# Kernel tuning notes

Hardware: AMD Instinct MI355X
Metric: run time of the kernel (lower is better)

The kernel has to match this reference:

```python
import jax, jax.numpy as jnp
import numpy as np

DIM = 2048
KV_DIM = 1024
NUM_HEADS = 16
HEAD_DIM = DIM // NUM_HEADS  # 128
EPS = 1e-6
B, LQ, LKV = 2, 4096, 1024


def _rope_cos_sin(L, d, base=10000.0):
    inv_freq = 1.0 / (base ** (np.arange(0, d, 2, dtype=np.float32) / d))  # [d/2]
    freqs = np.arange(L, dtype=np.float32)[:, None] * inv_freq[None, :]   # [L, d/2]
    emb = np.concatenate([freqs, freqs], axis=-1)                          # [L, d]
    return jnp.asarray(np.cos(emb)), jnp.asarray(np.sin(emb))


def setup_inputs() -> dict:
    key = jax.random.key(0)
    ks = jax.random.split(key, 10)
    x = jax.random.normal(ks[0], (B, LQ, DIM), dtype=jnp.float32)
    y = jax.random.normal(ks[1], (B, LKV, KV_DIM), dtype=jnp.float32)
    xc, xs = _rope_cos_sin(LQ, HEAD_DIM)
    yc, ys = _rope_cos_sin(LKV, HEAD_DIM)
    x_cos = jnp.broadcast_to(xc[None], (B, LQ, HEAD_DIM))
    x_sin = jnp.broadcast_to(xs[None], (B, LQ, HEAD_DIM))
    y_cos = jnp.broadcast_to(yc[None], (B, LKV, HEAD_DIM))
    y_sin = jnp.broadcast_to(ys[None], (B, LKV, HEAD_DIM))
    s = 0.02
    Wq = jax.random.normal(ks[2], (DIM, DIM), dtype=jnp.float32) * s
    Wk = jax.random.normal(ks[3], (DIM, KV_DIM), dtype=jnp.float32) * s
    Wv = jax.random.normal(ks[4], (DIM, KV_DIM), dtype=jnp.float32) * s
    Wo = jax.random.normal(ks[5], (DIM, DIM), dtype=jnp.float32) * s
    bq = jnp.zeros((DIM,), jnp.float32)
    bk = jnp.zeros((DIM,), jnp.float32)
    bv = jnp.zeros((DIM,), jnp.float32)
    bo = jnp.zeros((DIM,), jnp.float32)
    rmsq_w = jnp.ones((DIM,), jnp.float32)
    rmsk_w = jnp.ones((DIM,), jnp.float32)
    ln_w = jnp.ones((KV_DIM,), jnp.float32)
    ln_b = jnp.zeros((KV_DIM,), jnp.float32)
    return dict(x=x, y=y, x_cos=x_cos, x_sin=x_sin, y_cos=y_cos, y_sin=y_sin,
                Wq=Wq, bq=bq, Wk=Wk, bk=bk, Wv=Wv, bv=bv, Wo=Wo, bo=bo,
                rmsq_w=rmsq_w, rmsk_w=rmsk_w, ln_w=ln_w, ln_b=ln_b)


def _rms_norm(t, w, eps=EPS):
    return t * jax.lax.rsqrt(jnp.mean(t * t, axis=-1, keepdims=True) + eps) * w


def _layer_norm(t, w, b, eps=EPS):
    mu = jnp.mean(t, axis=-1, keepdims=True)
    var = jnp.mean(jnp.square(t - mu), axis=-1, keepdims=True)
    return (t - mu) * jax.lax.rsqrt(var + eps) * w + b


def _rotate_half(t):
    d2 = t.shape[-1] // 2
    return jnp.concatenate([-t[..., d2:], t[..., :d2]], axis=-1)


def _apply_rope(t, cos, sin):
    # t: [B, L, H, D]; cos/sin: [B, L, D] -> unsqueeze head dim (unsqueeze_dim=2)
    cos = cos[:, :, None, :]
    sin = sin[:, :, None, :]
    return t * cos + _rotate_half(t) * sin


def _block_forward(x, y, x_cos, x_sin, y_cos, y_sin,
                   Wq, bq, Wk, bk, Wv, bv, Wo, bo,
                   rmsq_w, rmsk_w, ln_w, ln_b):
    Bb, Lq, D = x.shape
    Lk = y.shape[1]
    H, Dh = NUM_HEADS, HEAD_DIM
    # y pre-norm (block-level LayerNorm)
    yn = _layer_norm(y, ln_w, ln_b)
    # projections + RMSNorm on q/k
    q = _rms_norm(x @ Wq.T + bq, rmsq_w)   # [B, Lq, D]
    k = _rms_norm(yn @ Wk.T + bk, rmsk_w)  # [B, Lk, D]
    v = yn @ Wv.T + bv                     # [B, Lk, D]
    # split heads and apply RoPE
    q = _apply_rope(q.reshape(Bb, Lq, H, Dh), x_cos, x_sin)
    k = _apply_rope(k.reshape(Bb, Lk, H, Dh), y_cos, y_sin)
    v = v.reshape(Bb, Lk, H, Dh)
    # non-causal cross attention, scale = 1/sqrt(head_dim)
    scale = 1.0 / jnp.sqrt(jnp.asarray(Dh, q.dtype))
    scores = jnp.einsum('blhd,bmhd->bhlm', q, k) * scale
    probs = jax.nn.softmax(scores, axis=-1)
    out = jnp.einsum('bhlm,bmhd->blhd', probs, v).reshape(Bb, Lq, D)
    return out @ Wo.T + bo


def reference(x, y, x_cos, x_sin, y_cos, y_sin,
              Wq, bq, Wk, bk, Wv, bv, Wo, bo,
              rmsq_w, rmsk_w, ln_w, ln_b):
    return _block_forward(x, y, x_cos, x_sin, y_cos, y_sin,
                          Wq, bq, Wk, bk, Wv, bv, Wo, bo,
                          rmsq_w, rmsk_w, ln_w, ln_b)
```

## Files before the change

### kernel.cpp

```cpp
#include <hip/hip_runtime.h>


typedef __attribute__((ext_vector_type(8))) short    short8;
typedef __attribute__((ext_vector_type(8))) unsigned short ushort8;
typedef __attribute__((ext_vector_type(4))) unsigned short ushort4v;
typedef __attribute__((ext_vector_type(4))) float    f32x4;
typedef __attribute__((ext_vector_type(2))) unsigned int uint2v;

#define DEV __device__ __forceinline__

DEV unsigned short f2bf(float f) {
  unsigned int u = __builtin_bit_cast(unsigned int, f);
  u += 0x7FFFu + ((u >> 16) & 1u);
  return (unsigned short)(u >> 16);
}
DEV float bf2f(unsigned short h) {
  return __builtin_bit_cast(float, ((unsigned int)h) << 16);
}
DEV unsigned int cvtpk_bf16(float lo, float hi) {
  unsigned int r;
  asm("v_cvt_pk_bf16_f32 %0, %1, %2" : "=v"(r) : "v"(lo), "v"(hi));
  return r;
}

DEV void gload_lds16(const void* g, void* l) {
  __builtin_amdgcn_global_load_lds(
      (const __attribute__((address_space(1))) void*)g,
      (__attribute__((address_space(3))) void*)l, 16, 0, 0);
}

__global__ __launch_bounds__(256) void cvt_kernel(const float* __restrict__ in,
                                                  unsigned short* __restrict__ out,
                                                  int n4) {
  int idx = blockIdx.x * 256 + threadIdx.x;
  int stride = gridDim.x * 256;
  for (int i = idx; i < n4; i += stride) {
    float4 v = *(const float4*)(in + (size_t)i * 4);
    ushort4v o;
    o.x = f2bf(v.x); o.y = f2bf(v.y); o.z = f2bf(v.z); o.w = f2bf(v.w);
    *(ushort4v*)(out + (size_t)i * 4) = o;
  }
}

__global__ __launch_bounds__(256) void ln_kernel(const float* __restrict__ y,
                                                 const float* __restrict__ w,
                                                 const float* __restrict__ b,
                                                 unsigned short* __restrict__ yn) {
  const int row = blockIdx.x;
  const int t = threadIdx.x;
  const float* yr = y + (size_t)row * 1024;
  float4 v = *(const float4*)(yr + t * 4);
  float s1 = v.x + v.y + v.z + v.w;
  float s2 = v.x * v.x + v.y * v.y + v.z * v.z + v.w * v.w;
#pragma unroll
  for (int m = 1; m < 64; m <<= 1) {
    s1 += __shfl_xor(s1, m);
    s2 += __shfl_xor(s2, m);
  }
  __shared__ float red[8];
  const int wave = t >> 6, lane = t & 63;
  if (lane == 0) { red[wave] = s1; red[4 + wave] = s2; }
  __syncthreads();
  s1 = red[0] + red[1] + red[2] + red[3];
  s2 = red[4] + red[5] + red[6] + red[7];
  const float mu = s1 * (1.0f / 1024.0f);
  const float var = s2 * (1.0f / 1024.0f) - mu * mu;
  const float rs = rsqrtf(var + 1e-6f);
  ushort4v o;
  o.x = f2bf((v.x - mu) * rs * w[t * 4 + 0] + b[t * 4 + 0]);
  o.y = f2bf((v.y - mu) * rs * w[t * 4 + 1] + b[t * 4 + 1]);
  o.z = f2bf((v.z - mu) * rs * w[t * 4 + 2] + b[t * 4 + 2]);
  o.w = f2bf((v.w - mu) * rs * w[t * 4 + 3] + b[t * 4 + 3]);
  *(ushort4v*)(yn + (size_t)row * 1024 + t * 4) = o;
}

__global__ __launch_bounds__(256) void gemm_bt(const unsigned short* __restrict__ A,
                                               const unsigned short* __restrict__ W,
                                               const float* __restrict__ bias0,
                                               const float* __restrict__ bias1,
                                               int nsplit,
                                               unsigned short* __restrict__ Cout,
                                               int M, int N, int K) {
  __shared__ __align__(16) char sA[128 * 128];
  __shared__ __align__(16) char sB[128 * 128];
  const int tid = threadIdx.x;
  const int wave = tid >> 6, lane = tid & 63;
  const int lg = lane >> 4, l15 = lane & 15;
  const int wr = wave >> 1, wc = wave & 1;
  const int m0 = blockIdx.y * 128;
  const int n0 = blockIdx.x * 128;
  const char* Ab = (const char*)A;
  const char* Wb = (const char*)W;
  const size_t ldab = (size_t)K * 2;

  f32x4 acc[4][4] = {};

  for (int kt = 0; kt < K; kt += 64) {
#pragma unroll
    for (int i = 0; i < 4; ++i) {
      const int p = (i * 256 + tid) * 16;
      const int row = p >> 7;
      const int si = (p & 127) ^ ((row & 7) << 4);
      gload_lds16(Ab + (size_t)(m0 + row) * ldab + (size_t)kt * 2 + si, sA + p);
    }
#pragma unroll
    for (int i = 0; i < 4; ++i) {
      const int p = (i * 256 + tid) * 16;
      const int row = p >> 7;
      const int si = (p & 127) ^ ((row & 7) << 4);
      gload_lds16(Wb + (size_t)(n0 + row) * ldab + (size_t)kt * 2 + si, sB + p);
    }
    __syncthreads();
#pragma unroll
    for (int ks = 0; ks < 2; ++ks) {
      const int kb = (ks * 32 + lg * 8) * 2;
      short8 af[4], bw[4];
#pragma unroll
      for (int mf = 0; mf < 4; ++mf) {
        const int row = wr * 64 + mf * 16 + l15;
        af[mf] = *(const short8*)(sA + row * 128 + (kb ^ ((row & 7) << 4)));
      }
#pragma unroll
      for (int nf = 0; nf < 4; ++nf) {
        const int row = wc * 64 + nf * 16 + l15;
        bw[nf] = *(const short8*)(sB + row * 128 + (kb ^ ((row & 7) << 4)));
      }
#pragma unroll
      for (int mf = 0; mf < 4; ++mf)
#pragma unroll
        for (int nf = 0; nf < 4; ++nf)
          acc[mf][nf] = __builtin_amdgcn_mfma_f32_16x16x32_bf16(af[mf], bw[nf],
                                                                acc[mf][nf], 0, 0, 0);
    }
    __syncthreads();
  }

#pragma unroll
  for (int nf = 0; nf < 4; ++nf) {
    const int n = n0 + wc * 64 + nf * 16 + l15;
    const float bv = (n < nsplit) ? bias0[n] : bias1[n - nsplit];
#pragma unroll
    for (int mf = 0; mf < 4; ++mf) {
      const int mB = m0 + wr * 64 + mf * 16 + lg * 4;
#pragma unroll
      for (int r = 0; r < 4; ++r)
        Cout[(size_t)(mB + r) * N + n] = f2bf(acc[mf][nf][r] + bv);
    }
  }
}

template <int EPI>
__global__ __launch_bounds__(512, 2) void gemm256(const unsigned short* __restrict__ A,
                                                  const unsigned short* __restrict__ W,
                                                  const float* __restrict__ bias,
                                                  void* __restrict__ Cout,
                                                  int M, int N, int K) {
  __shared__ __align__(16) char lds[2][4][16384];
  const int tid = threadIdx.x;
  const int wave = tid >> 6, lane = tid & 63;
  const int lg = lane >> 4, l15 = lane & 15;
  const int wm = wave >> 2, wn = wave & 3;

  const int nwg = gridDim.x;
  const int wgid = (blockIdx.x & 7) * (nwg >> 3) + (blockIdx.x >> 3);
  const int nbn = N >> 8;
  const int m0 = (wgid / nbn) * 256;
  const int n0 = (wgid % nbn) * 256;

  const char* Ab = (const char*)A;
  const char* Wb = (const char*)W;
  const size_t ld = (size_t)K * 2;
  const int NT = K >> 6;
  const int NI = NT >> 1;

  const int prow = tid >> 3;
  const int psw  = ((tid * 16) & 127) ^ ((prow & 7) << 4);
  const int pdst = tid * 16;
  const char* pAg = Ab + (size_t)(m0 + prow) * ld + psw;
  const char* pBg = Wb + (size_t)(n0 + prow) * ld + psw;

  f32x4 acc[8][4] = {};
  short8 af[4][2];
  short8 bf[4][2];

#define STG(BUF, HALF, ISB, TAU) do {                                         \
    const char* _g = ((ISB) ? pBg : pAg) + (size_t)(HALF) * 128 * ld +        \
                     (size_t)(TAU) * 128;                                     \
    char* _l = lds[BUF][(ISB) * 2 + (HALF)];                                  \
    gload_lds16(_g, _l + pdst);                                               \
    gload_lds16(_g + 64 * ld, _l + pdst + 8192);                              \
  } while (0)

#define LDA(BUF, H) do {                                                      \
    const char* _b = lds[BUF][wm];                                            \
    _Pragma("unroll") for (int mfl = 0; mfl < 4; ++mfl) {                     \
      const int _r = (H) * 64 + mfl * 16 + l15;                               \
      _Pragma("unroll") for (int ks = 0; ks < 2; ++ks)                        \
        af[mfl][ks] = *(const short8*)(_b + _r * 128 +                        \
                        ((ks * 64 + lg * 16) ^ ((_r & 7) << 4)));             \
    }                                                                         \
  } while (0)

#define LDB(BUF, G) do {                                                      \
    const char* _b = lds[BUF][2 + (wn >> 1)];                                 \
    _Pragma("unroll") for (int nfl = 0; nfl < 2; ++nfl) {                     \
      const int _r = (wn & 1) * 64 + (G) * 32 + nfl * 16 + l15;               \
      _Pragma("unroll") for (int ks = 0; ks < 2; ++ks)                        \
        bf[(G) * 2 + nfl][ks] = *(const short8*)(_b + _r * 128 +              \
                        ((ks * 64 + lg * 16) ^ ((_r & 7) << 4)));             \
    }                                                                         \
  } while (0)

#define MFMA_Q(H, G) do {                                                     \
    __builtin_amdgcn_s_setprio(1);                                            \
    _Pragma("unroll") for (int ks = 0; ks < 2; ++ks)                          \
    _Pragma("unroll") for (int mfl = 0; mfl < 4; ++mfl)                       \
    _Pragma("unroll") for (int nfl = 0; nfl < 2; ++nfl)                       \
      acc[(H) * 4 + mfl][(G) * 2 + nfl] =                                     \
        __builtin_amdgcn_mfma_f32_16x16x32_bf16(af[mfl][ks],                  \
            bf[(G) * 2 + nfl][ks], acc[(H) * 4 + mfl][(G) * 2 + nfl], 0,0,0); \
    __builtin_amdgcn_s_setprio(0);                                            \
  } while (0)

#define BAR() __builtin_amdgcn_s_barrier()
#define LGKM0() do { asm volatile("s_waitcnt lgkmcnt(0)" ::: "memory");       \
    __builtin_amdgcn_sched_barrier(0); } while (0)
#define VM4() asm volatile("s_waitcnt vmcnt(4)" ::: "memory")
#define VM0() asm volatile("s_waitcnt vmcnt(0)" ::: "memory")

  STG(0, 0, 0, 0); STG(0, 1, 0, 0); STG(0, 0, 1, 0); STG(0, 1, 1, 0);
  STG(1, 0, 1, 1); STG(1, 1, 1, 1);
  VM4(); BAR();

  for (int t = 0; t < NI - 1; ++t) {
    const int t2 = 2 * t;
    LDA(0, 0); LDB(0, 0); STG(1, 0, 0, t2 + 1);
    BAR(); LGKM0(); MFMA_Q(0, 0); BAR();
    LDB(0, 1); STG(1, 1, 0, t2 + 1);
    BAR(); LGKM0(); MFMA_Q(0, 1); BAR();
    LDA(0, 1); STG(0, 0, 1, t2 + 2);
    BAR(); LGKM0(); MFMA_Q(1, 1); BAR();
    STG(0, 1, 1, t2 + 2);
    BAR(); MFMA_Q(1, 0); VM4(); BAR();
    LDA(1, 0); LDB(1, 0); STG(0, 0, 0, t2 + 2);
    BAR(); LGKM0(); MFMA_Q(0, 0); BAR();
    LDB(1, 1); STG(0, 1, 0, t2 + 2);
    BAR(); LGKM0(); MFMA_Q(0, 1); BAR();
    LDA(1, 1); STG(1, 0, 1, t2 + 3);
    BAR(); LGKM0(); MFMA_Q(1, 1); BAR();
    STG(1, 1, 1, t2 + 3);
    BAR(); MFMA_Q(1, 0); VM4(); BAR();
  }

  LDA(0, 0); LDB(0, 0); STG(1, 0, 0, NT - 1);
  BAR(); LGKM0(); MFMA_Q(0, 0); BAR();
  LDB(0, 1); STG(1, 1, 0, NT - 1);
  BAR(); LGKM0(); MFMA_Q(0, 1); BAR();
  LDA(0, 1);
  BAR(); LGKM0(); MFMA_Q(1, 1); BAR();
  BAR(); MFMA_Q(1, 0); VM0(); BAR();
  LDA(1, 0); LDB(1, 0); LGKM0(); MFMA_Q(0, 0);
  LDB(1, 1); LGKM0(); MFMA_Q(0, 1);
  LDA(1, 1); LGKM0(); MFMA_Q(1, 1);
  MFMA_Q(1, 0);

#undef STG
#undef LDA
#undef LDB
#undef MFMA_Q
#undef BAR
#undef LGKM0
#undef VM4
#undef VM0

#pragma unroll
  for (int nf = 0; nf < 4; ++nf) {
    const int n = n0 + wn * 64 + nf * 16 + l15;
    const float bv = bias[n];
#pragma unroll
    for (int mf = 0; mf < 8; ++mf) {
      const int mB = m0 + wm * 128 + mf * 16 + lg * 4;
#pragma unroll
      for (int r = 0; r < 4; ++r) {
        const float v = acc[mf][nf][r] + bv;
        if constexpr (EPI == 0)
          ((unsigned short*)Cout)[(size_t)(mB + r) * N + n] = f2bf(v);
        else
          ((float*)Cout)[(size_t)(mB + r) * N + n] = v;
      }
    }
  }
}

__global__ __launch_bounds__(256) void rmsrope_kernel(const unsigned short* __restrict__ in,
                                                      const float* __restrict__ w,
                                                      const float* __restrict__ cs,
                                                      const float* __restrict__ sn,
                                                      unsigned short* __restrict__ out,
                                                      int L, int ldin, float scale) {
  const int row = blockIdx.x;
  const int t = threadIdx.x;
  __shared__ __align__(16) unsigned short srow[2048];
  __shared__ float red[4];
  const unsigned short* ir = in + (size_t)row * ldin;
  ushort8 v = *(const ushort8*)(ir + t * 8);
  float vals[8];
  float ss = 0.f;
#pragma unroll
  for (int j = 0; j < 8; ++j) { vals[j] = bf2f(v[j]); ss += vals[j] * vals[j]; }
  *(ushort8*)(srow + t * 8) = v;
#pragma unroll
  for (int m = 1; m < 64; m <<= 1) ss += __shfl_xor(ss, m);
  const int wave = t >> 6, lane = t & 63;
  if (lane == 0) red[wave] = ss;
  __syncthreads();
  const float tot = red[0] + red[1] + red[2] + red[3];
  const float rms = rsqrtf(tot * (1.0f / 2048.0f) + 1e-6f);

  const int n0 = t * 8;
  const int d0 = n0 & 127;
  const int hh = n0 >> 7;
  const float sign = (d0 < 64) ? -1.0f : 1.0f;
  const float* cb = cs + (size_t)row * 128 + d0;
  const float* sb = sn + (size_t)row * 128 + d0;
  ushort8 po = *(const ushort8*)(srow + (n0 ^ 64));
  ushort8 ou;
#pragma unroll
  for (int j = 0; j < 8; ++j) {
    const float self = vals[j] * rms * w[n0 + j];
    const float part = bf2f(po[j]) * rms * w[(n0 ^ 64) + j];
    ou[j] = f2bf((self * cb[j] + sign * part * sb[j]) * scale);
  }
  const int b = row / L, l = row - (row / L) * L;
  *(ushort8*)(out + (((size_t)(b * 16 + hh)) * L + l) * 128 + d0) = ou;
}

__global__ __launch_bounds__(256) void vtrans_kernel(const unsigned short* __restrict__ vpre,
                                                     unsigned short* __restrict__ vt,
                                                     int ldv) {
  const int bid = blockIdx.x;
  const int kt = bid & 15, bh = bid >> 4;
  const int h = bh & 15, b = bh >> 4;
  __shared__ unsigned short lt[64][130];
  const int t = threadIdx.x;
  const int i0 = t >> 4, c0 = (t & 15) * 8;
  const unsigned short* src = vpre + ((size_t)(b * 1024 + kt * 64)) * ldv + h * 128;
#pragma unroll
  for (int ii = 0; ii < 4; ++ii) {
    const int i = i0 + ii * 16;
    ushort8 v = *(const ushort8*)(src + (size_t)i * ldv + c0);
#pragma unroll
    for (int j = 0; j < 8; ++j) lt[i][c0 + j] = v[j];
  }
  __syncthreads();
  const int d0 = t >> 3, j0 = (t & 7) * 8;
  unsigned short* dst = vt + (size_t)bh * 128 * 1024 + kt * 64;
#pragma unroll
  for (int dd = 0; dd < 4; ++dd) {
    const int d = d0 + dd * 32;
    ushort8 o;
#pragma unroll
    for (int jj = 0; jj < 8; ++jj) o[jj] = lt[j0 + jj][d];
    *(ushort8*)(dst + (size_t)d * 1024 + j0) = o;
  }
}

__global__ __launch_bounds__(512, 2) void attn_kernel(const unsigned short* __restrict__ q,
                                                      const unsigned short* __restrict__ k,
                                                      const unsigned short* __restrict__ vt,
                                                      unsigned short* __restrict__ ao) {
  __shared__ __align__(16) char sK[2][64 * 256];
  __shared__ __align__(16) char sV[2][128 * 128];
  __shared__ __align__(16) char sP[8][32 * 64];

  const int bid = blockIdx.x;
  const int qt = bid & 15, bh = bid >> 4;
  const int tid = threadIdx.x;
  const int wave = tid >> 6, lane = tid & 63;
  const int lg = lane >> 4, l15 = lane & 15;

  const unsigned short* qbase = q + (((size_t)bh * 4096) + qt * 256 + wave * 32) * 128;
  const char* kbase = (const char*)(k + (size_t)bh * 1024 * 128);
  const char* vbase = (const char*)(vt + (size_t)bh * 128 * 1024);

  short8 qa[2][4];
#pragma unroll
  for (int mf = 0; mf < 2; ++mf)
#pragma unroll
    for (int ks = 0; ks < 4; ++ks)
      qa[mf][ks] = *(const short8*)(qbase + (size_t)(mf * 16 + l15) * 128 + ks * 32 + lg * 8);

  f32x4 o[2][8] = {};
  float lsum[2] = {0.f, 0.f};
  char* const pb = sP[wave];

#define STAGE_KV(BUF, KV0) do {                                              \
    _Pragma("unroll")                                                        \
    for (int i = 0; i < 2; ++i) {                                            \
      const int p = (i * 512 + tid) * 16;                                    \
      const int row = p >> 8;                                                \
      const int si = (p & 255) ^ ((row & 7) << 4);                           \
      gload_lds16(kbase + (size_t)((KV0) + row) * 256 + si, sK[BUF] + p);    \
    }                                                                        \
    _Pragma("unroll")                                                        \
    for (int i = 0; i < 2; ++i) {                                            \
      const int p = (i * 512 + tid) * 16;                                    \
      const int row = p >> 7;                                                \
      const int si = (p & 127) ^ ((row & 7) << 4);                           \
      gload_lds16(vbase + (size_t)row * 2048 + (KV0) * 2 + si, sV[BUF] + p); \
    }                                                                        \
  } while (0)

  STAGE_KV(0, 0);
  __syncthreads();

  int cur = 0;
  for (int kt = 0; kt < 16; ++kt) {
    if (kt < 15) STAGE_KV(cur ^ 1, (kt + 1) * 64);

    const char* const K = sK[cur];
    const char* const V = sV[cur];

#pragma unroll
    for (int hf = 0; hf < 2; ++hf) {
      f32x4 s[2][2] = {};
#pragma unroll
      for (int ks = 0; ks < 4; ++ks) {
        const int kb = ks * 64 + lg * 16;
#pragma unroll
        for (int fl = 0; fl < 2; ++fl) {
          const int krow = hf * 32 + fl * 16 + l15;
          short8 kf = *(const short8*)(K + krow * 256 + (kb ^ ((krow & 7) << 4)));
#pragma unroll
          for (int mf = 0; mf < 2; ++mf)
            s[fl][mf] = __builtin_amdgcn_mfma_f32_16x16x32_bf16(kf, qa[mf][ks],
                                                                s[fl][mf], 0, 0, 0);
        }
      }

#pragma unroll
      for (int mf = 0; mf < 2; ++mf) {
        const int prow = mf * 16 + l15;
        const int swz = (prow & 3) << 4;
#pragma unroll
        for (int fl = 0; fl < 2; ++fl) {
          const float p0 = exp2f(s[fl][mf][0]);
          const float p1 = exp2f(s[fl][mf][1]);
          const float p2 = exp2f(s[fl][mf][2]);
          const float p3 = exp2f(s[fl][mf][3]);
          lsum[mf] += (p0 + p1) + (p2 + p3);
          uint2v pw;
          pw.x = cvtpk_bf16(p0, p1);
          pw.y = cvtpk_bf16(p2, p3);
          *(uint2v*)(pb + prow * 64 + ((32 * fl + 8 * lg) ^ swz)) = pw;
        }
      }

      short8 pa[2];
#pragma unroll
      for (int mf = 0; mf < 2; ++mf) {
        const int prow = mf * 16 + l15;
        pa[mf] = *(const short8*)(pb + prow * 64 + ((lg * 16) ^ ((prow & 3) << 4)));
      }
      const int jb = hf * 64 + lg * 16;
#pragma unroll
      for (int nf = 0; nf < 8; ++nf) {
        const int vrow = nf * 16 + l15;
        short8 vf = *(const short8*)(V + vrow * 128 + (jb ^ ((vrow & 7) << 4)));
#pragma unroll
        for (int mf = 0; mf < 2; ++mf)
          o[mf][nf] = __builtin_amdgcn_mfma_f32_16x16x32_bf16(pa[mf], vf, o[mf][nf], 0, 0, 0);
      }
    }
    __syncthreads();
    cur ^= 1;
  }
#undef STAGE_KV

  float linv[2];
#pragma unroll
  for (int mf = 0; mf < 2; ++mf) {
    float t = lsum[mf];
    t += __shfl_xor(t, 16);
    t += __shfl_xor(t, 32);
    linv[mf] = 1.0f / t;
  }
  const int b = bh >> 4, h = bh & 15;
#pragma unroll
  for (int mf = 0; mf < 2; ++mf) {
#pragma unroll
    for (int r = 0; r < 4; ++r) {
      const float inv = __shfl(linv[mf], (lane & 48) | (lg * 4 + r));
      const int qg = qt * 256 + wave * 32 + mf * 16 + lg * 4 + r;
      const size_t orow = ((size_t)b * 4096 + qg) * 2048 + h * 128;
#pragma unroll
      for (int nf = 0; nf < 8; ++nf)
        ao[orow + nf * 16 + l15] = f2bf(o[mf][nf][r] * inv);
    }
  }
}

extern "C" void kernel_launch(void* const* d_in, const int* in_sizes, int n_in,
                              void* d_out, int out_size, void* d_ws, size_t ws_size,
                              hipStream_t stream) {
  (void)in_sizes; (void)n_in; (void)out_size; (void)ws_size;
  const float* x      = (const float*)d_in[0];
  const float* y      = (const float*)d_in[1];
  const float* x_cos  = (const float*)d_in[2];
  const float* x_sin  = (const float*)d_in[3];
  const float* y_cos  = (const float*)d_in[4];
  const float* y_sin  = (const float*)d_in[5];
  const float* Wq     = (const float*)d_in[6];
  const float* bq     = (const float*)d_in[7];
  const float* Wk     = (const float*)d_in[8];
  const float* bk     = (const float*)d_in[9];
  const float* Wv     = (const float*)d_in[10];
  const float* bv     = (const float*)d_in[11];
  const float* Wo     = (const float*)d_in[12];
  const float* bo     = (const float*)d_in[13];
  const float* rmsq_w = (const float*)d_in[14];
  const float* rmsk_w = (const float*)d_in[15];
  const float* ln_w   = (const float*)d_in[16];
  const float* ln_b   = (const float*)d_in[17];

  char* ws = (char*)d_ws;
  unsigned short* xb    = (unsigned short*)(ws + 0);
  unsigned short* Wqb   = (unsigned short*)(ws + 33554432);
  unsigned short* Wkb   = (unsigned short*)(ws + 41943040);
  unsigned short* Wvb   = (unsigned short*)(ws + 46137344);
  unsigned short* Wob   = (unsigned short*)(ws + 50331648);
  unsigned short* ynb   = (unsigned short*)(ws + 58720256);
  unsigned short* kvpre = (unsigned short*)(ws + 62914560);
  unsigned short* qpre  = (unsigned short*)(ws + 62914560);
  unsigned short* qr    = (unsigned short*)(ws + 96468992);
  unsigned short* kr    = (unsigned short*)(ws + 130023424);
  unsigned short* vt    = (unsigned short*)(ws + 138412032);
  unsigned short* ao    = xb;

  const float qscale = 1.4426950408889634f * 0.08838834764831843f;

  cvt_kernel<<<2048, 256, 0, stream>>>(x, xb, (2 * 4096 * 2048) / 4);
  cvt_kernel<<<512, 256, 0, stream>>>(Wq, Wqb, (2048 * 2048) / 4);
  cvt_kernel<<<512, 256, 0, stream>>>(Wk, Wkb, (2048 * 1024) / 4);
  cvt_kernel<<<512, 256, 0, stream>>>(Wv, Wvb, (2048 * 1024) / 4);
  cvt_kernel<<<512, 256, 0, stream>>>(Wo, Wob, (2048 * 2048) / 4);
  ln_kernel<<<2048, 256, 0, stream>>>(y, ln_w, ln_b, ynb);

  dim3 gKV(32, 16);
  gemm_bt<<<gKV, 256, 0, stream>>>(ynb, Wkb, bk, bv, 2048, kvpre, 2048, 4096, 1024);
  rmsrope_kernel<<<2048, 256, 0, stream>>>(kvpre, rmsk_w, y_cos, y_sin, kr, 1024, 4096, 1.0f);
  vtrans_kernel<<<512, 256, 0, stream>>>(kvpre + 2048, vt, 4096);

  gemm256<0><<<256, 512, 0, stream>>>(xb, Wqb, bq, qpre, 8192, 2048, 2048);
  rmsrope_kernel<<<8192, 256, 0, stream>>>(qpre, rmsq_w, x_cos, x_sin, qr, 4096, 2048, qscale);

  attn_kernel<<<512, 512, 0, stream>>>(qr, kr, vt, ao);

  gemm256<1><<<256, 512, 0, stream>>>(ao, Wob, bo, (float*)d_out, 8192, 2048, 2048);
}
```

Measured before the change: 329.5 us.

## Switch attention to 32x32x16 MFMA with register-resident P via lane shuffles

```diff
diff --git a/kernel.cpp b/kernel.cpp
--- a/kernel.cpp
+++ b/kernel.cpp
@@ -5,7 +5,8 @@
 typedef __attribute__((ext_vector_type(8))) unsigned short ushort8;
 typedef __attribute__((ext_vector_type(4))) unsigned short ushort4v;
 typedef __attribute__((ext_vector_type(4))) float    f32x4;
-typedef __attribute__((ext_vector_type(2))) unsigned int uint2v;
+typedef __attribute__((ext_vector_type(16))) float   f32x16;
+typedef __attribute__((ext_vector_type(4))) unsigned int uint4v;
 
 #define DEV __device__ __forceinline__
 
@@ -21,6 +22,10 @@
   unsigned int r;
   asm("v_cvt_pk_bf16_f32 %0, %1, %2" : "=v"(r) : "v"(lo), "v"(hi));
   return r;
+}
+DEV short8 mk8(unsigned a, unsigned b, unsigned c, unsigned d) {
+  uint4v t; t.x = a; t.y = b; t.z = c; t.w = d;
+  return __builtin_bit_cast(short8, t);
 }
 
 DEV void gload_lds16(const void* g, void* l) {
@@ -371,28 +376,26 @@
                                                       unsigned short* __restrict__ ao) {
   __shared__ __align__(16) char sK[2][64 * 256];
   __shared__ __align__(16) char sV[2][128 * 128];
-  __shared__ __align__(16) char sP[8][32 * 64];
-
-  const int bid = blockIdx.x;
+
+  const int bid0 = blockIdx.x;
+  const int bid = (bid0 & 7) * 64 + (bid0 >> 3);
   const int qt = bid & 15, bh = bid >> 4;
   const int tid = threadIdx.x;
   const int wave = tid >> 6, lane = tid & 63;
-  const int lg = lane >> 4, l15 = lane & 15;
+  const int l31 = lane & 31, hi = lane >> 5;
+  const bool hib = (hi != 0);
 
   const unsigned short* qbase = q + (((size_t)bh * 4096) + qt * 256 + wave * 32) * 128;
   const char* kbase = (const char*)(k + (size_t)bh * 1024 * 128);
   const char* vbase = (const char*)(vt + (size_t)bh * 128 * 1024);
 
-  short8 qa[2][4];
-#pragma unroll
-  for (int mf = 0; mf < 2; ++mf)
-#pragma unroll
-    for (int ks = 0; ks < 4; ++ks)
-      qa[mf][ks] = *(const short8*)(qbase + (size_t)(mf * 16 + l15) * 128 + ks * 32 + lg * 8);
-
-  f32x4 o[2][8] = {};
-  float lsum[2] = {0.f, 0.f};
-  char* const pb = sP[wave];
+  short8 qb[8];
+#pragma unroll
+  for (int step = 0; step < 8; ++step)
+    qb[step] = *(const short8*)(qbase + (size_t)l31 * 128 + step * 16 + hi * 8);
+
+  f32x16 o[4] = {};
+  float lsum = 0.f;
 
 #define STAGE_KV(BUF, KV0) do {                                              \
     _Pragma("unroll")                                                        \
@@ -411,6 +414,37 @@
     }                                                                        \
   } while (0)
 
+#define SOFTMAX_PV(SS, F) do {                                               \
+    float p_[16];                                                            \
+    _Pragma("unroll") for (int r = 0; r < 16; ++r) p_[r] = exp2f((SS)[r]);   \
+    lsum += ((p_[0]+p_[1])+(p_[2]+p_[3])) + ((p_[4]+p_[5])+(p_[6]+p_[7]))    \
+          + ((p_[8]+p_[9])+(p_[10]+p_[11])) + ((p_[12]+p_[13])+(p_[14]+p_[15]));\
+    const unsigned w0 = cvtpk_bf16(p_[0], p_[1]),  w1 = cvtpk_bf16(p_[2], p_[3]), \
+                   w2 = cvtpk_bf16(p_[4], p_[5]),  w3 = cvtpk_bf16(p_[6], p_[7]), \
+                   w4 = cvtpk_bf16(p_[8], p_[9]),  w5 = cvtpk_bf16(p_[10], p_[11]),\
+                   w6 = cvtpk_bf16(p_[12], p_[13]),w7 = cvtpk_bf16(p_[14], p_[15]);\
+    const unsigned x0 = (unsigned)__shfl_xor((int)(hib ? w0 : w2), 32);      \
+    const unsigned x1 = (unsigned)__shfl_xor((int)(hib ? w1 : w3), 32);      \
+    const unsigned x2 = (unsigned)__shfl_xor((int)(hib ? w4 : w6), 32);      \
+    const unsigned x3 = (unsigned)__shfl_xor((int)(hib ? w5 : w7), 32);      \
+    const short8 fr0 = mk8(hib ? x0 : w0, hib ? x1 : w1,                     \
+                           hib ? w2 : x0, hib ? w3 : x1);                    \
+    const short8 fr1 = mk8(hib ? x2 : w4, hib ? x3 : w5,                     \
+                           hib ? w6 : x2, hib ? w7 : x3);                    \
+    __builtin_amdgcn_s_setprio(1);                                           \
+    _Pragma("unroll") for (int kstep = 0; kstep < 2; ++kstep) {              \
+      const short8 pa = kstep ? fr1 : fr0;                                   \
+      const int col = (F) * 64 + kstep * 32 + hi * 16;                       \
+      _Pragma("unroll") for (int dt = 0; dt < 4; ++dt) {                     \
+        const int vrow = dt * 32 + l31;                                      \
+        short8 vf = *(const short8*)(V + vrow * 128 +                        \
+                                     (col ^ ((vrow & 7) << 4)));             \
+        o[dt] = __builtin_amdgcn_mfma_f32_32x32x16_bf16(pa, vf, o[dt], 0,0,0);\
+      }                                                                      \
+    }                                                                        \
+    __builtin_amdgcn_s_setprio(0);                                           \
+  } while (0)
+
   STAGE_KV(0, 0);
   __syncthreads();
 
@@ -421,82 +455,41 @@
     const char* const K = sK[cur];
     const char* const V = sV[cur];
 
-#pragma unroll
-    for (int hf = 0; hf < 2; ++hf) {
-      f32x4 s[2][2] = {};
-#pragma unroll
-      for (int ks = 0; ks < 4; ++ks) {
-        const int kb = ks * 64 + lg * 16;
-#pragma unroll
-        for (int fl = 0; fl < 2; ++fl) {
-          const int krow = hf * 32 + fl * 16 + l15;
-          short8 kf = *(const short8*)(K + krow * 256 + (kb ^ ((krow & 7) << 4)));
-#pragma unroll
-          for (int mf = 0; mf < 2; ++mf)
-            s[fl][mf] = __builtin_amdgcn_mfma_f32_16x16x32_bf16(kf, qa[mf][ks],
-                                                                s[fl][mf], 0, 0, 0);
-        }
-      }
-
-#pragma unroll
-      for (int mf = 0; mf < 2; ++mf) {
-        const int prow = mf * 16 + l15;
-        const int swz = (prow & 3) << 4;
-#pragma unroll
-        for (int fl = 0; fl < 2; ++fl) {
-          const float p0 = exp2f(s[fl][mf][0]);
-          const float p1 = exp2f(s[fl][mf][1]);
-          const float p2 = exp2f(s[fl][mf][2]);
-          const float p3 = exp2f(s[fl][mf][3]);
-          lsum[mf] += (p0 + p1) + (p2 + p3);
-          uint2v pw;
-          pw.x = cvtpk_bf16(p0, p1);
-          pw.y = cvtpk_bf16(p2, p3);
-          *(uint2v*)(pb + prow * 64 + ((32 * fl + 8 * lg) ^ swz)) = pw;
-        }
-      }
-
-      short8 pa[2];
-#pragma unroll
-      for (int mf = 0; mf < 2; ++mf) {
-        const int prow = mf * 16 + l15;
-        pa[mf] = *(const short8*)(pb + prow * 64 + ((lg * 16) ^ ((prow & 3) << 4)));
-      }
-      const int jb = hf * 64 + lg * 16;
-#pragma unroll
-      for (int nf = 0; nf < 8; ++nf) {
-        const int vrow = nf * 16 + l15;
-        short8 vf = *(const short8*)(V + vrow * 128 + (jb ^ ((vrow & 7) << 4)));
-#pragma unroll
-        for (int mf = 0; mf < 2; ++mf)
-          o[mf][nf] = __builtin_amdgcn_mfma_f32_16x16x32_bf16(pa[mf], vf, o[mf][nf], 0, 0, 0);
-      }
+    f32x16 s0 = {}, s1 = {};
+    const int krow0 = l31, krow1 = 32 + l31;
+    const int ksw0 = (krow0 & 7) << 4, ksw1 = (krow1 & 7) << 4;
+    __builtin_amdgcn_s_setprio(1);
+#pragma unroll
+    for (int step = 0; step < 8; ++step) {
+      const int cb2 = step * 32 + hi * 16;
+      short8 kf0 = *(const short8*)(K + krow0 * 256 + (cb2 ^ ksw0));
+      short8 kf1 = *(const short8*)(K + krow1 * 256 + (cb2 ^ ksw1));
+      s0 = __builtin_amdgcn_mfma_f32_32x32x16_bf16(kf0, qb[step], s0, 0, 0, 0);
+      s1 = __builtin_amdgcn_mfma_f32_32x32x16_bf16(kf1, qb[step], s1, 0, 0, 0);
     }
+    __builtin_amdgcn_s_setprio(0);
+
+    SOFTMAX_PV(s0, 0);
+    SOFTMAX_PV(s1, 1);
+
     __syncthreads();
     cur ^= 1;
   }
 #undef STAGE_KV
-
-  float linv[2];
-#pragma unroll
-  for (int mf = 0; mf < 2; ++mf) {
-    float t = lsum[mf];
-    t += __shfl_xor(t, 16);
-    t += __shfl_xor(t, 32);
-    linv[mf] = 1.0f / t;
-  }
+#undef SOFTMAX_PV
+
+  lsum += __shfl_xor(lsum, 32);
+  const float linv = 1.0f / lsum;
   const int b = bh >> 4, h = bh & 15;
 #pragma unroll
-  for (int mf = 0; mf < 2; ++mf) {
-#pragma unroll
-    for (int r = 0; r < 4; ++r) {
-      const float inv = __shfl(linv[mf], (lane & 48) | (lg * 4 + r));
-      const int qg = qt * 256 + wave * 32 + mf * 16 + lg * 4 + r;
-      const size_t orow = ((size_t)b * 4096 + qg) * 2048 + h * 128;
-#pragma unroll
-      for (int nf = 0; nf < 8; ++nf)
-        ao[orow + nf * 16 + l15] = f2bf(o[mf][nf][r] * inv);
-    }
+  for (int r = 0; r < 16; ++r) {
+    const int crow = (r & 3) + 8 * (r >> 2) + 4 * hi;
+    const float inv = __shfl(linv, crow);
+    const int qg = qt * 256 + wave * 32 + crow;
+    const size_t orow = ((size_t)b * 4096 + qg) * 2048 + h * 128;
+#pragma unroll
+    for (int dt = 0; dt < 4; ++dt)
+      ao[orow + dt * 32 + l31] = f2bf(o[dt][r] * inv);
   }
 }
 
```

Result: no change. 325.8 us (-1.1%).
